# Performance work log

Measured on AMD Instinct MI355X. Metric: run time of the kernel, lower is better.

## Reference

```python
import jax, jax.numpy as jnp
import numpy as np

N_QUBITS = 10
DEPTH = 5
DIM = 2 ** N_QUBITS  # 1024
NUM_CLASSES = 2
BATCH = 16384
IN_DIM = 784


def _rot_matrices(w):
    # w: [depth, n_qubits, 3] angles (phi, theta, omega); qml.Rot = RZ(omega) RY(theta) RZ(phi)
    phi, theta, omega = w[..., 0], w[..., 1], w[..., 2]
    c, s = jnp.cos(theta / 2), jnp.sin(theta / 2)
    e = lambda a: jnp.exp(1j * a.astype(jnp.complex64))
    m00 = e(-(phi + omega) / 2) * c
    m01 = -e((phi - omega) / 2) * s
    m10 = e(-(phi - omega) / 2) * s
    m11 = e((phi + omega) / 2) * c
    return jnp.stack([jnp.stack([m00, m01], -1), jnp.stack([m10, m11], -1)], -2)  # [D, n, 2, 2]


def _apply_1q(state, U, w):
    # state: [B] + [2]*n ; apply 2x2 U on qubit axis w
    s = jnp.moveaxis(state, w + 1, -1)
    s = s @ U.T
    return jnp.moveaxis(s, -1, w + 1)


def _apply_cnot(state, c, t):
    s = jnp.moveaxis(state, (c + 1, t + 1), (-2, -1))
    s = jnp.concatenate([s[..., 0:1, :], s[..., 1:2, ::-1]], axis=-2)  # flip target where control=1
    return jnp.moveaxis(s, (-2, -1), (c + 1, t + 1))


def _circuit(x, weights):
    B = x.shape[0]
    # AmplitudeEmbedding: pad_with=0, normalize=True
    amp = jnp.pad(x, ((0, 0), (0, DIM - x.shape[1])))
    amp = amp / jnp.linalg.norm(amp, axis=1, keepdims=True)
    state = amp.astype(jnp.complex64).reshape((B,) + (2,) * N_QUBITS)
    U = _rot_matrices(weights)
    for d in range(DEPTH):
        for i in range(N_QUBITS):  # entangling CNOT ring
            state = _apply_cnot(state, i, (i + 1) % N_QUBITS)
        for i in range(N_QUBITS):  # per-qubit Rot
            state = _apply_1q(state, U[d, i], i)
    probs = (state.real ** 2 + state.imag ** 2).reshape(B, DIM)
    # <Z_i> = P(bit_i = 0) - P(bit_i = 1)
    z = []
    for i in range(N_QUBITS):
        p = probs.reshape(B, 2 ** i, 2, -1)
        z.append(p[:, :, 0, :].sum((1, 2)) - p[:, :, 1, :].sum((1, 2)))
    return jnp.stack(z, axis=1)  # [B, n_qubits]


def setup_inputs() -> dict:
    key = jax.random.key(0)
    k1, k2, k3 = jax.random.split(key, 3)
    x = jax.random.normal(k1, (BATCH, IN_DIM), dtype=jnp.float32)
    weights = jax.random.uniform(k2, (DEPTH, N_QUBITS, 3), dtype=jnp.float32) * (2.0 * np.pi)
    y = jax.random.randint(k3, (BATCH,), 0, NUM_CLASSES)
    return {"x": x, "weights": weights, "y": y}


def reference(x, weights, y):
    logits = _circuit(x, weights)[:, :NUM_CLASSES]
    logp = jax.nn.log_softmax(logits, axis=-1)
    loss = -jnp.take_along_axis(logp, y[:, None], axis=1).mean()
    return loss
```

## Files before the change

### kernel.cpp

```cpp
#include <hip/hip_runtime.h>
#include <type_traits>

#define NQ 10
#define N_DEPTH 5
#define DIM 1024
#define BATCH 16384
#define IN_DIM 784
#define NGATES 50
#define KALLOC 832
#define NT 13
#define NSLOT 768
#define NB 6

typedef float f32x2 __attribute__((ext_vector_type(2)));
typedef float f32x4 __attribute__((ext_vector_type(4)));
typedef unsigned u32x4 __attribute__((ext_vector_type(4)));

struct MaskTab {
  unsigned v[NGATES];
  unsigned p[NGATES];
  unsigned vz0, vz1;
};

constexpr MaskTab make_masks() {
  MaskTab t{};
  unsigned v[NQ], p[NQ];
  for (int i = 0; i < NQ; ++i) { v[i] = 1u << (9 - i); p[i] = 1u << (9 - i); }
  for (int d = 0; d < N_DEPTH; ++d) {
    for (int i = 0; i < NQ; ++i) {
      int c = i, tt = (i + 1) % NQ;
      v[tt] ^= v[c];
      p[c]  ^= p[tt];
    }
    for (int i = 0; i < NQ; ++i) {
      t.v[d * NQ + i] = v[i];
      t.p[d * NQ + i] = p[i];
    }
  }
  t.vz0 = v[0];
  t.vz1 = v[1];
  return t;
}

constexpr MaskTab MT = make_masks();
__constant__ MaskTab d_MT = make_masks();

struct PermTab { short slot[DIM]; };
constexpr PermTab make_perm() {
  PermTab t{};
  int a = 0, b = 256, c = 512;
  for (int m = 0; m < DIM; ++m) {
    const int p0 = __builtin_popcount((unsigned)m & MT.vz0) & 1;
    const int p1 = __builtin_popcount((unsigned)m & MT.vz1) & 1;
    if (p0 && !p1)      t.slot[m] = (short)a++;
    else if (!p0 && p1) t.slot[m] = (short)b++;
    else if (p0 && p1)  t.slot[m] = (short)c++;
    else                t.slot[m] = -1;
  }
  return t;
}
__constant__ PermTab d_PT = make_perm();

__device__ __forceinline__ f32x2 ampfma(f32x2 o, f32x2 q, f32x2 co, f32x2 cp) {
  f32x2 d;
  asm("v_pk_mul_f32 %0, %2, %1 op_sel:[0,0] op_sel_hi:[0,1]\n\t"
      "v_pk_fma_f32 %0, %2, %1, %0 op_sel:[1,1,0] op_sel_hi:[1,0,1] neg_lo:[1,0,0]\n\t"
      "v_pk_fma_f32 %0, %3, %4, %0 op_sel:[0,0,0] op_sel_hi:[0,1,1]\n\t"
      "v_pk_fma_f32 %0, %3, %4, %0 op_sel:[1,1,0] op_sel_hi:[1,0,1] neg_lo:[1,0,0]"
      : "=&v"(d)
      : "v"(o), "v"(co), "v"(cp), "v"(q));
  return d;
}

__device__ __forceinline__ float fxor(float x, unsigned m) {
  return __uint_as_float(__float_as_uint(x) ^ m);
}

__device__ __forceinline__ unsigned pk4_fp8(float a, float b, float c, float d) {
  int v = __builtin_amdgcn_cvt_pk_fp8_f32(a, b, 0, false);
  v = __builtin_amdgcn_cvt_pk_fp8_f32(c, d, v, true);
  return (unsigned)v;
}

__device__ __forceinline__ void gll16(const void* g, void* l) {
  __builtin_amdgcn_global_load_lds(
      (const __attribute__((address_space(1))) void*)g,
      (__attribute__((address_space(3))) void*)l, 16, 0, 0);
}

#define XSCALE 32.0f
#define WSCALE 16.0f
#define SINV   (1.0f / 262144.0f)

__global__ __launch_bounds__(256) void prep(const float* __restrict__ X,
                                            char* __restrict__ Xf8,
                                            float* __restrict__ xn2,
                                            const float* __restrict__ w,
                                            unsigned short* __restrict__ W2u) {
  __shared__ f32x4 UL4[NGATES];
  __shared__ f32x2 S0[DIM];
  __shared__ f32x2 S1[DIM];

  const int tid = threadIdx.x;

  if (blockIdx.x >= 832) {
    const int row = (blockIdx.x - 832) * 8 + (tid >> 5);
    const int l32 = tid & 31;
    const float* src = X + (size_t)row * IN_DIM;
    char* dst = Xf8 + (size_t)row * KALLOC;
    float ssq = 0.0f;
    for (int c = l32; c < 52; c += 32) {
      u32x4 out;
      if (c < 49) {
        f32x4 v0 = *(const f32x4*)(src + c * 16);
        f32x4 v1 = *(const f32x4*)(src + c * 16 + 4);
        f32x4 v2 = *(const f32x4*)(src + c * 16 + 8);
        f32x4 v3 = *(const f32x4*)(src + c * 16 + 12);
        ssq += v0.x * v0.x + v0.y * v0.y + v0.z * v0.z + v0.w * v0.w +
               v1.x * v1.x + v1.y * v1.y + v1.z * v1.z + v1.w * v1.w +
               v2.x * v2.x + v2.y * v2.y + v2.z * v2.z + v2.w * v2.w +
               v3.x * v3.x + v3.y * v3.y + v3.z * v3.z + v3.w * v3.w;
        out = u32x4{
          pk4_fp8(v0.x * XSCALE, v0.y * XSCALE, v0.z * XSCALE, v0.w * XSCALE),
          pk4_fp8(v1.x * XSCALE, v1.y * XSCALE, v1.z * XSCALE, v1.w * XSCALE),
          pk4_fp8(v2.x * XSCALE, v2.y * XSCALE, v2.z * XSCALE, v2.w * XSCALE),
          pk4_fp8(v3.x * XSCALE, v3.y * XSCALE, v3.z * XSCALE, v3.w * XSCALE)};
      } else {
        out = u32x4{0, 0, 0, 0};
      }
      *(u32x4*)(dst + c * 16) = out;
    }
#pragma unroll
    for (int off = 1; off < 32; off <<= 1) ssq += __shfl_xor(ssq, off);
    if (l32 == 0) xn2[row] = ssq;
    return;
  }

  if (tid < NGATES) {
    float phi = w[tid * 3 + 0], th = w[tid * 3 + 1], om = w[tid * 3 + 2];
    float ct = cosf(th * 0.5f), st = sinf(th * 0.5f);
    float aa = (phi + om) * 0.5f, bb = (phi - om) * 0.5f;
    float cA = cosf(aa), sA = sinf(aa), cB = cosf(bb), sB = sinf(bb);
    UL4[tid] = f32x4{ ct * cA, -ct * sA, -st * cB, -st * sB };
  }

  const int j = blockIdx.x;
  unsigned short* rowp = W2u + (size_t)j * NSLOT;

  if (j >= IN_DIM) {
#pragma unroll
    for (int k = 0; k < 3; ++k) rowp[tid + k * 256] = 0;
    return;
  }

#pragma unroll
  for (int k = 0; k < 4; ++k) {
    const int m = tid + k * 256;
    S0[m] = f32x2{(m == j) ? 1.0f : 0.0f, 0.0f};
  }
  __syncthreads();

  for (int g = 0; g < NGATES; ++g) {
    const f32x2* src = (g & 1) ? S1 : S0;
    f32x2* dst = (g & 1) ? S0 : S1;
    const f32x4 A = UL4[g];
    const unsigned v = d_MT.v[g];
    const unsigned p = d_MT.p[g];
#pragma unroll
    for (int k = 0; k < 4; ++k) {
      const int m = tid + k * 256;
      f32x2 o = src[m];
      f32x2 q = src[m ^ (int)p];
      const unsigned sg = (unsigned)(__popc((int)((unsigned)m & v)) & 1) << 31;
      const f32x2 co = {A.x, fxor(A.y, sg)};
      const f32x2 cp = {fxor(A.z, sg), A.w};
      dst[m] = ampfma(o, q, co, cp);
    }
    __syncthreads();
  }

  const f32x2* fin = S0;
#pragma unroll
  for (int k = 0; k < 4; ++k) {
    const int m = tid + k * 256;
    const int s = d_PT.slot[m];
    f32x2 a = fin[m];
    if (s >= 0)
      rowp[s] = (unsigned short)(pk4_fp8(a.x * WSCALE, a.y * WSCALE,
                                         0.0f, 0.0f) & 0xffffu);
  }
}

__global__ __launch_bounds__(256) void transpose_w(const unsigned* __restrict__ W2u32,
                                                   unsigned* __restrict__ W2Tu32) {
  __shared__ unsigned tile[64][33];
  const int j0 = blockIdx.x * 64;
  const int s0 = blockIdx.y * 64;
  const int t = threadIdx.x;
#pragma unroll
  for (int i = 0; i < 8; ++i) {
    const int idx = i * 256 + t;
    const int jr = idx >> 5, sc = idx & 31;
    tile[jr][sc] = W2u32[(size_t)(j0 + jr) * (NSLOT / 2) + (s0 >> 1) + sc];
  }
  __syncthreads();
#pragma unroll
  for (int i = 0; i < 8; ++i) {
    const int idx = i * 256 + t;
    const int rl = idx >> 4, jq = idx & 15;
    const int slot = rl >> 1, c = rl & 1;
    const int sc = slot >> 1, p = slot & 1;
    unsigned out = 0;
#pragma unroll
    for (int q = 0; q < 4; ++q) {
      const unsigned w32 = tile[jq * 4 + q][sc];
      const unsigned h = (w32 >> (16 * p)) & 0xffffu;
      out |= ((h >> (8 * c)) & 0xffu) << (8 * q);
    }
    const int orow = 2 * (s0 + slot) + c;
    W2Tu32[((size_t)orow * KALLOC + j0 + jq * 4) >> 2] = out;
  }
}

__global__ __launch_bounds__(512) void gemm_fused(const char* __restrict__ Xf8,
                                                  const char* __restrict__ W2T,
                                                  float* __restrict__ accb) {
  __shared__ u32x4 lds4[4096];
  char* lds = (char*)lds4;

  const int tid = threadIdx.x;
  const int orig = blockIdx.x;
  const int bx = (orig & 7) * 48 + (orig >> 3);
  const int mb = bx / NB, nb = bx % NB;
  const int m0 = mb * 256, n0 = nb * 256;
  const int lane = tid & 63, wv = tid >> 6;
  const int wm = wv >> 2, wn = wv & 3;

  const int rl = lane >> 2;
  const int csrc = (lane & 3) ^ (rl & 3) ^ ((rl >> 2) & 3);

  auto stage = [&](int t) {
    char* Ab = lds + (t & 1) * 32768;
    char* Bb = Ab + 16384;
    const int col = t * 64 + csrc * 16;
#pragma unroll
    for (int i = 0; i < 2; ++i) {
      const int g = wv * 2 + i;
      const int row = g * 16 + rl;
      gll16(Xf8 + (size_t)(m0 + row) * KALLOC + col, Ab + g * 1024);
    }
#pragma unroll
    for (int i = 0; i < 2; ++i) {
      const int g = wv * 2 + i;
      const int row = g * 16 + rl;
      gll16(W2T + (size_t)(n0 + row) * KALLOC + col, Bb + g * 1024);
    }
  };

  stage(0);
  asm volatile("s_waitcnt vmcnt(0)" ::: "memory");
  __builtin_amdgcn_s_barrier();

  f32x4 acc[8][4];
#pragma unroll
  for (int fm = 0; fm < 8; ++fm)
#pragma unroll
    for (int fn = 0; fn < 4; ++fn) acc[fm][fn] = f32x4{0, 0, 0, 0};

  const int kc = lane >> 4;

  for (int t = 0; t < NT; ++t) {
    const char* Ab = lds + (t & 1) * 32768;
    const char* Bb = Ab + 16384;

    long af0[8], bf0[4], af1[8], bf1[4];
#pragma unroll
    for (int f = 0; f < 8; ++f) {
      const int ar = wm * 128 + f * 16 + (lane & 15);
      const int sw = (ar & 3) ^ ((ar >> 2) & 3);
      af0[f] = *(const long*)(Ab + ar * 64 + (((kc >> 1) ^ sw) * 16) + (kc & 1) * 8);
    }
#pragma unroll
    for (int f = 0; f < 4; ++f) {
      const int br = wn * 64 + f * 16 + (lane & 15);
      const int sw = (br & 3) ^ ((br >> 2) & 3);
      bf0[f] = *(const long*)(Bb + br * 64 + (((kc >> 1) ^ sw) * 16) + (kc & 1) * 8);
    }
    if (t < NT - 1) stage(t + 1);
#pragma unroll
    for (int f = 0; f < 8; ++f) {
      const int ar = wm * 128 + f * 16 + (lane & 15);
      const int sw = (ar & 3) ^ ((ar >> 2) & 3);
      const int kb = 4 + kc;
      af1[f] = *(const long*)(Ab + ar * 64 + (((kb >> 1) ^ sw) * 16) + (kb & 1) * 8);
    }
#pragma unroll
    for (int f = 0; f < 4; ++f) {
      const int br = wn * 64 + f * 16 + (lane & 15);
      const int sw = (br & 3) ^ ((br >> 2) & 3);
      const int kb = 4 + kc;
      bf1[f] = *(const long*)(Bb + br * 64 + (((kb >> 1) ^ sw) * 16) + (kb & 1) * 8);
    }

    __builtin_amdgcn_s_setprio(1);
#pragma unroll
    for (int fm = 0; fm < 8; ++fm)
#pragma unroll
      for (int fn = 0; fn < 4; ++fn)
        acc[fm][fn] = __builtin_amdgcn_mfma_f32_16x16x32_fp8_fp8(
            af0[fm], bf0[fn], acc[fm][fn], 0, 0, 0);
    __builtin_amdgcn_s_setprio(0);

    __builtin_amdgcn_s_setprio(1);
#pragma unroll
    for (int fm = 0; fm < 8; ++fm)
#pragma unroll
      for (int fn = 0; fn < 4; ++fn)
        acc[fm][fn] = __builtin_amdgcn_mfma_f32_16x16x32_fp8_fp8(
            af1[fm], bf1[fn], acc[fm][fn], 0, 0, 0);
    __builtin_amdgcn_s_setprio(0);

    if (t < NT - 1) {
      asm volatile("s_waitcnt vmcnt(0)" ::: "memory");
      __builtin_amdgcn_sched_barrier(0);
      __builtin_amdgcn_s_barrier();
    }
  }

#pragma unroll
  for (int fm = 0; fm < 8; ++fm) {
    float sn[4] = {0, 0, 0, 0};
#pragma unroll
    for (int fn = 0; fn < 4; ++fn) {
#pragma unroll
      for (int r = 0; r < 4; ++r) {
        const float vv = acc[fm][fn][r];
        sn[r] = fmaf(vv, vv, sn[r]);
      }
    }
#pragma unroll
    for (int off = 1; off < 16; off <<= 1) {
#pragma unroll
      for (int r = 0; r < 4; ++r) sn[r] += __shfl_xor(sn[r], off);
    }
    if ((lane & 15) == 0) {
#pragma unroll
      for (int r = 0; r < 4; ++r) {
        const int m = m0 + wm * 128 + fm * 16 + (lane >> 4) * 4 + r;
        accb[(size_t)nb * BATCH + m] = sn[r];
      }
    }
  }
}

__global__ __launch_bounds__(256) void loss_partial(const float* __restrict__ accb,
                                                    const float* __restrict__ xn2,
                                                    const int* __restrict__ y,
                                                    float* __restrict__ partial) {
  const int s = blockIdx.x * 256 + threadIdx.x;
  const float SA = (accb[0 * BATCH + s] + accb[1 * BATCH + s]) * SINV;
  const float SB = (accb[2 * BATCH + s] + accb[3 * BATCH + s]) * SINV;
  const float SC = (accb[4 * BATCH + s] + accb[5 * BATCH + s]) * SINV;
  const float n2 = xn2[s];
  const float z0 = n2 - 2.0f * (SA + SC);
  const float z1 = n2 - 2.0f * (SB + SC);
  const float inv = 1.0f / n2;
  const float l0 = z0 * inv, l1 = z1 * inv;
  const float mx = fmaxf(l0, l1);
  const float lse = mx + logf(expf(l0 - mx) + expf(l1 - mx));
  float loss = lse - ((y[s] == 0) ? l0 : l1);

  __shared__ float sm[256];
  sm[threadIdx.x] = loss;
  __syncthreads();
  for (int st = 128; st > 0; st >>= 1) {
    if (threadIdx.x < st) sm[threadIdx.x] += sm[threadIdx.x + st];
    __syncthreads();
  }
  if (threadIdx.x == 0) partial[blockIdx.x] = sm[0];
}

__global__ __launch_bounds__(64) void loss_final(const float* __restrict__ partial,
                                                 float* __restrict__ out) {
  float v = partial[threadIdx.x];
#pragma unroll
  for (int off = 1; off < 64; off <<= 1) v += __shfl_xor(v, off);
  if (threadIdx.x == 0) out[0] = v * (1.0f / (float)BATCH);
}

extern "C" void kernel_launch(void* const* d_in, const int* in_sizes, int n_in,
                              void* d_out, int out_size, void* d_ws, size_t ws_size,
                              hipStream_t stream) {
  const float* x = (const float*)d_in[0];
  const float* w = (const float*)d_in[1];
  const int*   y = (const int*)d_in[2];

  char* ws = (char*)d_ws;
  char*     Xf8  = ws;
  unsigned short* W2u = (unsigned short*)(ws + 13631488);
  char*     W2Tu = ws + 14909440;
  float*    xn2  = (float*)(ws + 16187392);
  float*    accb = (float*)(ws + 16252928);
  float* partial = (float*)(ws + 16646144);

  prep<<<2880, 256, 0, stream>>>(x, Xf8, xn2, w, W2u);
  transpose_w<<<dim3(13, 12), 256, 0, stream>>>((const unsigned*)W2u,
                                                (unsigned*)W2Tu);
  gemm_fused<<<384, 512, 0, stream>>>(Xf8, W2Tu, accb);
  loss_partial<<<BATCH / 256, 256, 0, stream>>>(accb, xn2, y, partial);
  loss_final<<<1, 64, 0, stream>>>(partial, (float*)d_out);
}
```

Before: 87.42 us.

## Write transposed weights directly in prep and halve GEMM N-tile

Result: faster. 79.10 us (-9.5%).

```diff
diff --git a/kernel.cpp b/kernel.cpp
--- a/kernel.cpp
+++ b/kernel.cpp
@@ -10,7 +10,7 @@
 #define KALLOC 832
 #define NT 13
 #define NSLOT 768
-#define NB 6
+#define NB 12
 
 typedef float f32x2 __attribute__((ext_vector_type(2)));
 typedef float f32x4 __attribute__((ext_vector_type(4)));
@@ -96,7 +96,7 @@
                                             char* __restrict__ Xf8,
                                             float* __restrict__ xn2,
                                             const float* __restrict__ w,
-                                            unsigned short* __restrict__ W2u) {
+                                            char* __restrict__ W2T) {
   __shared__ f32x4 UL4[NGATES];
   __shared__ f32x2 S0[DIM];
   __shared__ f32x2 S1[DIM];
@@ -145,11 +145,14 @@
   }
 
   const int j = blockIdx.x;
-  unsigned short* rowp = W2u + (size_t)j * NSLOT;
 
   if (j >= IN_DIM) {
 #pragma unroll
-    for (int k = 0; k < 3; ++k) rowp[tid + k * 256] = 0;
+    for (int k = 0; k < 3; ++k) {
+      const int s = tid + k * 256;
+      W2T[(size_t)(2 * s) * KALLOC + j] = 0;
+      W2T[(size_t)(2 * s + 1) * KALLOC + j] = 0;
+    }
     return;
   }
 
@@ -185,54 +188,25 @@
     const int m = tid + k * 256;
     const int s = d_PT.slot[m];
     f32x2 a = fin[m];
-    if (s >= 0)
-      rowp[s] = (unsigned short)(pk4_fp8(a.x * WSCALE, a.y * WSCALE,
-                                         0.0f, 0.0f) & 0xffffu);
-  }
-}
-
-__global__ __launch_bounds__(256) void transpose_w(const unsigned* __restrict__ W2u32,
-                                                   unsigned* __restrict__ W2Tu32) {
-  __shared__ unsigned tile[64][33];
-  const int j0 = blockIdx.x * 64;
-  const int s0 = blockIdx.y * 64;
-  const int t = threadIdx.x;
-#pragma unroll
-  for (int i = 0; i < 8; ++i) {
-    const int idx = i * 256 + t;
-    const int jr = idx >> 5, sc = idx & 31;
-    tile[jr][sc] = W2u32[(size_t)(j0 + jr) * (NSLOT / 2) + (s0 >> 1) + sc];
-  }
-  __syncthreads();
-#pragma unroll
-  for (int i = 0; i < 8; ++i) {
-    const int idx = i * 256 + t;
-    const int rl = idx >> 4, jq = idx & 15;
-    const int slot = rl >> 1, c = rl & 1;
-    const int sc = slot >> 1, p = slot & 1;
-    unsigned out = 0;
-#pragma unroll
-    for (int q = 0; q < 4; ++q) {
-      const unsigned w32 = tile[jq * 4 + q][sc];
-      const unsigned h = (w32 >> (16 * p)) & 0xffffu;
-      out |= ((h >> (8 * c)) & 0xffu) << (8 * q);
-    }
-    const int orow = 2 * (s0 + slot) + c;
-    W2Tu32[((size_t)orow * KALLOC + j0 + jq * 4) >> 2] = out;
+    if (s >= 0) {
+      const unsigned pk = pk4_fp8(a.x * WSCALE, a.y * WSCALE, 0.0f, 0.0f);
+      W2T[(size_t)(2 * s) * KALLOC + j] = (char)(pk & 0xffu);
+      W2T[(size_t)(2 * s + 1) * KALLOC + j] = (char)((pk >> 8) & 0xffu);
+    }
   }
 }
 
 __global__ __launch_bounds__(512) void gemm_fused(const char* __restrict__ Xf8,
                                                   const char* __restrict__ W2T,
                                                   float* __restrict__ accb) {
-  __shared__ u32x4 lds4[4096];
+  __shared__ u32x4 lds4[3072];
   char* lds = (char*)lds4;
 
   const int tid = threadIdx.x;
   const int orig = blockIdx.x;
-  const int bx = (orig & 7) * 48 + (orig >> 3);
+  const int bx = (orig & 7) * 96 + (orig >> 3);
   const int mb = bx / NB, nb = bx % NB;
-  const int m0 = mb * 256, n0 = nb * 256;
+  const int m0 = mb * 256, n0 = nb * 128;
   const int lane = tid & 63, wv = tid >> 6;
   const int wm = wv >> 2, wn = wv & 3;
 
@@ -240,7 +214,7 @@
   const int csrc = (lane & 3) ^ (rl & 3) ^ ((rl >> 2) & 3);
 
   auto stage = [&](int t) {
-    char* Ab = lds + (t & 1) * 32768;
+    char* Ab = lds + (t & 1) * 24576;
     char* Bb = Ab + 16384;
     const int col = t * 64 + csrc * 16;
 #pragma unroll
@@ -249,11 +223,9 @@
       const int row = g * 16 + rl;
       gll16(Xf8 + (size_t)(m0 + row) * KALLOC + col, Ab + g * 1024);
     }
-#pragma unroll
-    for (int i = 0; i < 2; ++i) {
-      const int g = wv * 2 + i;
-      const int row = g * 16 + rl;
-      gll16(W2T + (size_t)(n0 + row) * KALLOC + col, Bb + g * 1024);
+    {
+      const int row = wv * 16 + rl;
+      gll16(W2T + (size_t)(n0 + row) * KALLOC + col, Bb + wv * 1024);
     }
   };
 
@@ -261,19 +233,19 @@
   asm volatile("s_waitcnt vmcnt(0)" ::: "memory");
   __builtin_amdgcn_s_barrier();
 
-  f32x4 acc[8][4];
+  f32x4 acc[8][2];
 #pragma unroll
   for (int fm = 0; fm < 8; ++fm)
 #pragma unroll
-    for (int fn = 0; fn < 4; ++fn) acc[fm][fn] = f32x4{0, 0, 0, 0};
+    for (int fn = 0; fn < 2; ++fn) acc[fm][fn] = f32x4{0, 0, 0, 0};
 
   const int kc = lane >> 4;
 
   for (int t = 0; t < NT; ++t) {
-    const char* Ab = lds + (t & 1) * 32768;
+    const char* Ab = lds + (t & 1) * 24576;
     const char* Bb = Ab + 16384;
 
-    long af0[8], bf0[4], af1[8], bf1[4];
+    long af0[8], bf0[2], af1[8], bf1[2];
 #pragma unroll
     for (int f = 0; f < 8; ++f) {
       const int ar = wm * 128 + f * 16 + (lane & 15);
@@ -281,8 +253,8 @@
       af0[f] = *(const long*)(Ab + ar * 64 + (((kc >> 1) ^ sw) * 16) + (kc & 1) * 8);
     }
 #pragma unroll
-    for (int f = 0; f < 4; ++f) {
-      const int br = wn * 64 + f * 16 + (lane & 15);
+    for (int f = 0; f < 2; ++f) {
+      const int br = wn * 32 + f * 16 + (lane & 15);
       const int sw = (br & 3) ^ ((br >> 2) & 3);
       bf0[f] = *(const long*)(Bb + br * 64 + (((kc >> 1) ^ sw) * 16) + (kc & 1) * 8);
     }
@@ -295,8 +267,8 @@
       af1[f] = *(const long*)(Ab + ar * 64 + (((kb >> 1) ^ sw) * 16) + (kb & 1) * 8);
     }
 #pragma unroll
-    for (int f = 0; f < 4; ++f) {
-      const int br = wn * 64 + f * 16 + (lane & 15);
+    for (int f = 0; f < 2; ++f) {
+      const int br = wn * 32 + f * 16 + (lane & 15);
       const int sw = (br & 3) ^ ((br >> 2) & 3);
       const int kb = 4 + kc;
       bf1[f] = *(const long*)(Bb + br * 64 + (((kb >> 1) ^ sw) * 16) + (kb & 1) * 8);
@@ -306,7 +278,7 @@
 #pragma unroll
     for (int fm = 0; fm < 8; ++fm)
 #pragma unroll
-      for (int fn = 0; fn < 4; ++fn)
+      for (int fn = 0; fn < 2; ++fn)
         acc[fm][fn] = __builtin_amdgcn_mfma_f32_16x16x32_fp8_fp8(
             af0[fm], bf0[fn], acc[fm][fn], 0, 0, 0);
     __builtin_amdgcn_s_setprio(0);
@@ -315,7 +287,7 @@
 #pragma unroll
     for (int fm = 0; fm < 8; ++fm)
 #pragma unroll
-      for (int fn = 0; fn < 4; ++fn)
+      for (int fn = 0; fn < 2; ++fn)
         acc[fm][fn] = __builtin_amdgcn_mfma_f32_16x16x32_fp8_fp8(
             af1[fm], bf1[fn], acc[fm][fn], 0, 0, 0);
     __builtin_amdgcn_s_setprio(0);
@@ -331,7 +303,7 @@
   for (int fm = 0; fm < 8; ++fm) {
     float sn[4] = {0, 0, 0, 0};
 #pragma unroll
-    for (int fn = 0; fn < 4; ++fn) {
+    for (int fn = 0; fn < 2; ++fn) {
 #pragma unroll
       for (int r = 0; r < 4; ++r) {
         const float vv = acc[fm][fn][r];
@@ -358,9 +330,14 @@
                                                     const int* __restrict__ y,
                                                     float* __restrict__ partial) {
   const int s = blockIdx.x * 256 + threadIdx.x;
-  const float SA = (accb[0 * BATCH + s] + accb[1 * BATCH + s]) * SINV;
-  const float SB = (accb[2 * BATCH + s] + accb[3 * BATCH + s]) * SINV;
-  const float SC = (accb[4 * BATCH + s] + accb[5 * BATCH + s]) * SINV;
+  float SA = 0.0f, SB = 0.0f, SC = 0.0f;
+#pragma unroll
+  for (int k = 0; k < 4; ++k) {
+    SA += accb[(size_t)(0 + k) * BATCH + s];
+    SB += accb[(size_t)(4 + k) * BATCH + s];
+    SC += accb[(size_t)(8 + k) * BATCH + s];
+  }
+  SA *= SINV; SB *= SINV; SC *= SINV;
   const float n2 = xn2[s];
   const float z0 = n2 - 2.0f * (SA + SC);
   const float z1 = n2 - 2.0f * (SB + SC);
@@ -397,16 +374,13 @@
 
   char* ws = (char*)d_ws;
   char*     Xf8  = ws;
-  unsigned short* W2u = (unsigned short*)(ws + 13631488);
-  char*     W2Tu = ws + 14909440;
-  float*    xn2  = (float*)(ws + 16187392);
-  float*    accb = (float*)(ws + 16252928);
-  float* partial = (float*)(ws + 16646144);
-
-  prep<<<2880, 256, 0, stream>>>(x, Xf8, xn2, w, W2u);
-  transpose_w<<<dim3(13, 12), 256, 0, stream>>>((const unsigned*)W2u,
-                                                (unsigned*)W2Tu);
-  gemm_fused<<<384, 512, 0, stream>>>(Xf8, W2Tu, accb);
+  char*     W2Tu = ws + 13631488;
+  float*    xn2  = (float*)(ws + 14909440);
+  float*    accb = (float*)(ws + 14975232);
+  float* partial = (float*)(ws + 15761408);
+
+  prep<<<2880, 256, 0, stream>>>(x, Xf8, xn2, w, W2Tu);
+  gemm_fused<<<768, 512, 0, stream>>>(Xf8, W2Tu, accb);
   loss_partial<<<BATCH / 256, 256, 0, stream>>>(accb, xn2, y, partial);
   loss_final<<<1, 64, 0, stream>>>(partial, (float*)d_out);
 }
```
